# Performance work log

Measured on AMD Instinct MI355X. Metric: run time of the kernel, lower is better.

The kernel has to match this reference:

```python
import jax, jax.numpy as jnp
import numpy as np

HEADS, DIM_HEAD, K_NN, EMB = 4, 64, 16, 256
INNER = HEADS * DIM_HEAD  # 256
POS_HID = 64
ATTN_HID = 4 * DIM_HEAD  # per-head hidden of grouped 1x1 conv MLP


def setup_inputs() -> dict:
    key = jax.random.key(0)
    ks = jax.random.split(key, 16)
    b, n = 2, 4096
    s = 0.05
    inp = {
        "x": jax.random.normal(ks[0], (b, n, EMB), jnp.float32),
        "mask": jnp.ones((b, n), dtype=bool),
        "pos": jax.random.normal(ks[1], (b, n, 3), jnp.float32),
        # to_qkv (no bias)
        "Wqkv": jax.random.normal(ks[2], (EMB, 3 * INNER), jnp.float32) * s,
        # pos_mlp: Linear(3,64) -> ReLU -> Linear(64, inner)
        "Wp1": jax.random.normal(ks[3], (3, POS_HID), jnp.float32) * s,
        "bp1": jax.random.normal(ks[4], (POS_HID,), jnp.float32) * s,
        "Wp2": jax.random.normal(ks[5], (POS_HID, INNER), jnp.float32) * s,
        "bp2": jax.random.normal(ks[6], (INNER,), jnp.float32) * s,
        # attn_mlp: grouped 1x1 convs == per-head linears [h, d_in, d_out]
        "Wa1": jax.random.normal(ks[7], (HEADS, DIM_HEAD, ATTN_HID), jnp.float32) * s,
        "ba1": jax.random.normal(ks[8], (HEADS, ATTN_HID), jnp.float32) * s,
        "Wa2": jax.random.normal(ks[9], (HEADS, ATTN_HID, DIM_HEAD), jnp.float32) * s,
        "ba2": jax.random.normal(ks[10], (HEADS, DIM_HEAD), jnp.float32) * s,
        # to_out
        "Wo": jax.random.normal(ks[11], (INNER, EMB), jnp.float32) * s,
        "bo": jax.random.normal(ks[12], (EMB,), jnp.float32) * s,
    }
    return inp


def reference(x, mask, pos, Wqkv, Wp1, bp1, Wp2, bp2, Wa1, ba1, Wa2, ba2, Wo, bo):
    b, n, _ = x.shape
    h, dh = HEADS, DIM_HEAD

    qkv = x @ Wqkv                              # [b, n, 3*inner]
    q, k, v = jnp.split(qkv, 3, axis=-1)
    to_heads = lambda t: t.reshape(b, n, h, dh).transpose(0, 2, 1, 3)  # [b,h,n,d]
    q, k, v = to_heads(q), to_heads(k), to_heads(v)

    # kNN on pos (per batch, squared euclidean, includes self)
    sq = jnp.sum(pos * pos, axis=-1)
    d2 = sq[:, :, None] + sq[:, None, :] - 2.0 * jnp.einsum('bid,bjd->bij', pos, pos)
    idx = jax.lax.top_k(-d2, K_NN)[1]            # [b, n, K]

    gat_h = jax.vmap(lambda t, i: t[:, i])       # [h,n,d],[n,K] -> [h,n,K,d]
    gat = jax.vmap(lambda t, i: t[i])            # [n,c],[n,K]  -> [n,K,c]

    qg = gat_h(q, idx)                           # [b,h,n,K,d]
    kg = gat_h(k, idx)
    vg = gat_h(v, idx)

    rel = gat(pos, idx) - pos[:, :, None, :]     # [b,n,K,3]
    rpe = jax.nn.relu(rel @ Wp1 + bp1) @ Wp2 + bp2               # [b,n,K,inner]
    rpe = rpe.reshape(b, n, K_NN, h, dh).transpose(0, 3, 1, 2, 4)  # [b,h,n,K,d]

    attn_in = qg - kg + rpe                      # [b,h,n,K,d]
    hid = jax.nn.relu(jnp.einsum('bhnkd,hde->bhnke', attn_in, Wa1)
                      + ba1[None, :, None, None, :])
    sim = (jnp.einsum('bhnke,hed->bhnkd', hid, Wa2)
           + ba2[None, :, None, None, :])        # [b,h,n,K,d]

    mg = jax.vmap(lambda m, i: m[i])(mask, idx)  # [b,n,K]
    pair = (mask[:, :, None] & mg)[:, None, :, :, None]
    sim = jnp.where(pair, sim, -jnp.finfo(sim.dtype).max)

    attn = jax.nn.softmax(sim, axis=3)           # over neighbors j
    # F.normalize over dim=-2 of [b,(h d),i,j] == over the point axis i
    attn = attn / jnp.maximum(jnp.linalg.norm(attn, axis=2, keepdims=True), 1e-12)

    agg = jnp.sum(attn * (vg + rpe), axis=3)     # [b,h,n,d]
    agg = agg.transpose(0, 2, 1, 3).reshape(b, n, h * dh)
    return agg @ Wo + bo
```

## Files before the change

kernel.cpp:

```cpp
#include <hip/hip_runtime.h>
#include <float.h>

typedef unsigned int uint;
typedef unsigned short ushort;

typedef _Float16 f16x8 __attribute__((ext_vector_type(8)));
typedef float f32x4 __attribute__((ext_vector_type(4)));
#define MFMA_F16(A, B, C) __builtin_amdgcn_mfma_f32_16x16x32_f16(A, B, C, 0, 0, 0)

__device__ __forceinline__ ushort f2h(float f) {
    _Float16 h = (_Float16)f;
    return __builtin_bit_cast(ushort, h);
}
__device__ __forceinline__ float h2f(ushort u) {
    _Float16 h = __builtin_bit_cast(_Float16, u);
    return (float)h;
}
__device__ __forceinline__ uint pack2(float a, float b) {
    return (uint)f2h(a) | ((uint)f2h(b) << 16);
}
__device__ __forceinline__ uint pkrtz(float a, float b) {
    return __builtin_bit_cast(uint, __builtin_amdgcn_cvt_pkrtz(a, b));
}
__device__ __forceinline__ f16x8 cast8(uint4 u) {
    return __builtin_bit_cast(f16x8, u);
}

template <int CTRL>
__device__ __forceinline__ void dpp_min(float& v, int& j) {
    int vp = __builtin_amdgcn_update_dpp(__float_as_int(v), __float_as_int(v),
                                         CTRL, 0xF, 0xF, false);
    int jp = __builtin_amdgcn_update_dpp(j, j, CTRL, 0xF, 0xF, false);
    float vf = __int_as_float(vp);
    bool better = (vf < v) || (vf == v && jp < j);
    v = better ? vf : v;
    j = better ? jp : j;
}
__device__ __forceinline__ void wave_min(float& v, int& j) {
    dpp_min<0x121>(v, j);
    dpp_min<0x122>(v, j);
    dpp_min<0x124>(v, j);
    dpp_min<0x128>(v, j);
    float ov = __shfl_xor(v, 16);
    int oj = __shfl_xor(j, 16);
    bool better = (ov < v) || (ov == v && oj < j);
    v = better ? ov : v;
    j = better ? oj : j;
    ov = __shfl_xor(v, 32);
    oj = __shfl_xor(j, 32);
    better = (ov < v) || (ov == v && oj < j);
    v = better ? ov : v;
    j = better ? oj : j;
}

__global__ void prep_kernel(const float* __restrict__ Wqkv, const float* __restrict__ Wa1,
                            const float* __restrict__ Wa2, const float* __restrict__ Wo,
                            const float* __restrict__ Wp2, const float* __restrict__ ba1,
                            ushort* __restrict__ WcatT, ushort* __restrict__ Wa1T,
                            ushort* __restrict__ Wa2T, ushort* __restrict__ WoT,
                            ushort* __restrict__ Wp2T, ushort* __restrict__ ba1p) {
    int t = blockIdx.x * 256 + threadIdx.x;
    {
        int cc2 = t >> 8, kk = t & 255;
        float val;
        if (cc2 < 256) val = Wqkv[kk * 768 + cc2] - Wqkv[kk * 768 + 256 + cc2];
        else           val = Wqkv[kk * 768 + 256 + cc2];
        WcatT[t] = f2h(val);
    }
    if (t < 65536) {
        int hh = t >> 14, r = t & 16383;
        int e = r >> 6, kin = r & 63;
        Wa1T[t] = f2h(Wa1[((size_t)(hh * 64 + kin)) * 256 + e]);
        int d = r >> 8, pos = r & 255;
        int ec = pos >> 5, lg = (pos >> 3) & 3, q = pos & 7;
        int e2 = ec * 32 + ((q >> 2) & 1) * 16 + lg * 4 + (q & 3);
        Wa2T[t] = f2h(Wa2[((size_t)(hh * 256 + e2)) * 64 + d]);
        int c3 = t >> 8, k3 = t & 255;
        WoT[t] = f2h(Wo[k3 * 256 + c3]);
    }
    if (t < 16384) {
        int row = t >> 6, p = t & 63;
        int h = row >> 6, s = row & 63;
        int ct = s >> 4, rr = s & 15;
        int d = (ct >> 1) * 32 + ((rr >> 2) & 3) * 8 + (ct & 1) * 4 + (rr & 3);
        Wp2T[t] = f2h(Wp2[p * 256 + h * 64 + d]);
    }
    if (t < 1024) {
        int h = t >> 8, pos = t & 255;
        int ec = pos >> 5, lg = (pos >> 3) & 3, q = pos & 7;
        int e2 = ec * 32 + ((q >> 2) & 1) * 16 + lg * 4 + (q & 3);
        ba1p[t] = f2h(ba1[h * 256 + e2]);
    }
}

__global__ void pos4_kernel(const float* __restrict__ pos, float4* __restrict__ pos4) {
    int t = blockIdx.x * 256 + threadIdx.x;
    float x = pos[t * 3 + 0], y = pos[t * 3 + 1], z = pos[t * 3 + 2];
    float4 o = {x, y, z, x * x + y * y + z * z};
    pos4[t] = o;
}

template <int MODE>
__global__ __launch_bounds__(256)
void hgemm(const void* __restrict__ Av, const ushort* __restrict__ Bt,
           const float* __restrict__ bias, void* __restrict__ C0v, ushort* __restrict__ C1h) {
    __shared__ ushort Af[64 * 40];
    __shared__ ushort Bf[128 * 40];
    const int tid = threadIdx.x;
    const int l = tid & 63, wv = tid >> 6;
    const int lg = l >> 4, lr = l & 15;
    const int row0 = blockIdx.x * 64, col0 = blockIdx.y * 128;
    const int mrow = (wv >> 1) * 32, ncol = (wv & 1) * 64;
    f32x4 acc[2][4];
#pragma unroll
    for (int mt = 0; mt < 2; ++mt)
#pragma unroll
        for (int nt = 0; nt < 4; ++nt) acc[mt][nt] = (f32x4){0.f, 0.f, 0.f, 0.f};

    for (int kk = 0; kk < 256; kk += 32) {
        if (MODE == 0) {
            const float* A = (const float*)Av;
            int r = tid >> 2, kq = (tid & 3) * 8;
            float4 a0 = *(const float4*)&A[(size_t)(row0 + r) * 256 + kk + kq];
            float4 a1 = *(const float4*)&A[(size_t)(row0 + r) * 256 + kk + kq + 4];
            uint4 u;
            u.x = pack2(a0.x, a0.y); u.y = pack2(a0.z, a0.w);
            u.z = pack2(a1.x, a1.y); u.w = pack2(a1.z, a1.w);
            *(uint4*)&Af[r * 40 + kq] = u;
        } else {
            const ushort* Ah = (const ushort*)Av;
            int r = tid >> 2, kq = (tid & 3) * 8;
            *(uint4*)&Af[r * 40 + kq] = *(const uint4*)&Ah[(size_t)(row0 + r) * 256 + kk + kq];
        }
        {
            int r = tid >> 1, hh = (tid & 1) * 16;
            const uint4* src = (const uint4*)&Bt[(size_t)(col0 + r) * 256 + kk + hh];
            uint4 b0 = src[0], b1 = src[1];
            *(uint4*)&Bf[r * 40 + hh] = b0;
            *(uint4*)&Bf[r * 40 + hh + 8] = b1;
        }
        __syncthreads();
        f16x8 afr[2], bfr[4];
#pragma unroll
        for (int mt = 0; mt < 2; ++mt)
            afr[mt] = *(const f16x8*)&Af[(mrow + mt * 16 + lr) * 40 + lg * 8];
#pragma unroll
        for (int nt = 0; nt < 4; ++nt)
            bfr[nt] = *(const f16x8*)&Bf[(ncol + nt * 16 + lr) * 40 + lg * 8];
#pragma unroll
        for (int mt = 0; mt < 2; ++mt)
#pragma unroll
            for (int nt = 0; nt < 4; ++nt)
                acc[mt][nt] = MFMA_F16(afr[mt], bfr[nt], acc[mt][nt]);
        __syncthreads();
    }
#pragma unroll
    for (int mt = 0; mt < 2; ++mt)
#pragma unroll
        for (int nt = 0; nt < 4; ++nt)
#pragma unroll
            for (int j = 0; j < 4; ++j) {
                int m = row0 + mrow + mt * 16 + lg * 4 + j;
                int n = col0 + ncol + nt * 16 + lr;
                float v = acc[mt][nt][j];
                if (MODE == 1) {
                    ((float*)C0v)[(size_t)m * 256 + n] = v + bias[n];
                } else {
                    int b = m >> 12, i2 = m & 4095;
                    if (n < 256) {
                        int hh = n >> 6, d = n & 63;
                        ((ushort*)C0v)[((size_t)((b * 4 + hh) << 12) + i2) * 64 + d] = f2h(v);
                    } else {
                        int n2 = n - 256;
                        int hh = n2 >> 6, d = n2 & 63;
                        C1h[((size_t)((b * 4 + hh) << 12) + i2) * 64 + d] = f2h(v);
                    }
                }
            }
}

__global__ __launch_bounds__(256, 6)
void knn_kernel(const float4* __restrict__ pos4, int* __restrict__ idx_out) {
    const int tid = threadIdx.x;
    const int lane = tid & 63, wv = tid >> 6;
    const int pblk = blockIdx.x;
    const int b = pblk >> 10;
    const int i = ((pblk & 1023) << 2) + wv;
    const float4* p4 = pos4 + (size_t)b * 4096;
    float4 pi = p4[i];
    float xi = pi.x, yi = pi.y, zi = pi.z, sqi = pi.w;

    float cm4[4];
    int cj4[4];
#pragma unroll
    for (int g = 0; g < 4; ++g) { cm4[g] = FLT_MAX; cj4[g] = 0x7fffffff; }
#pragma unroll 4
    for (int m = 0; m < 64; ++m) {
        int j = m * 64 + lane;
        float4 pj = p4[j];
        float v = sqi + pj.w - 2.f * (xi * pj.x + yi * pj.y + zi * pj.z);
        int g = m & 3;
        bool better = (v < cm4[g]) || (v == cm4[g] && j < cj4[g]);
        cm4[g] = better ? v : cm4[g];
        cj4[g] = better ? j : cj4[g];
    }
    float cm = cm4[0];
    int cj = cj4[0];
#pragma unroll
    for (int g = 1; g < 4; ++g) {
        bool better = (cm4[g] < cm) || (cm4[g] == cm && cj4[g] < cj);
        cm = better ? cm4[g] : cm;
        cj = better ? cj4[g] : cj;
    }

    unsigned long long extr = 0ull;
    int keep = 0;
#pragma unroll 1
    for (int r = 0; r < 16; ++r) {
        float bv = cm;
        int bj = cj;
        wave_min(bv, bj);
        if (lane == r) keep = bj;
        int c = bj & 63;
        int j = lane * 64 + c;
        float4 pj = p4[j];
        float v = sqi + pj.w - 2.f * (xi * pj.x + yi * pj.y + zi * pj.z);
        bool dead = (((extr >> c) & 1ull) != 0ull) | (j == bj);
        if (j == bj) extr |= (1ull << c);
        v = dead ? FLT_MAX : v;
        int nj = j;
        wave_min(v, nj);
        if (lane == c) { cm = v; cj = nj; }
    }
    if (lane < 16)
        idx_out[((size_t)b * 4096 + i) * 16 + lane] = keep;
}

__global__ __launch_bounds__(256)
void attn_mfma(const ushort* __restrict__ qmkh, const ushort* __restrict__ vbufh,
               const float4* __restrict__ pos4, const int* __restrict__ idxb,
               const ushort* __restrict__ Wa1Tg, const ushort* __restrict__ Wa2Tg,
               const ushort* __restrict__ Wp2Tg, const ushort* __restrict__ ba1p,
               const float* __restrict__ ba2,
               const float* __restrict__ Wp1, const float* __restrict__ bp1,
               const float* __restrict__ bp2,
               ushort* __restrict__ prodbuf, float* __restrict__ part) {
    __shared__ ushort scr[4][16 * 88];
    const int tid = threadIdx.x;
    const int l = tid & 63, wv = tid >> 6;
    const int lg = l >> 4, lr = l & 15;
    const int c = blockIdx.x;
    const int h = c >> 8, rc = c & 255, b = rc >> 7, chunk = rc & 127;
    const int bh = b * 4 + h;

    const ushort* w1g = Wa1Tg + (size_t)h * 16384;
    const ushort* w2g = Wa2Tg + (size_t)h * 16384;

    float b2v[4];
#pragma unroll
    for (int dt = 0; dt < 4; ++dt) b2v[dt] = ba2[h * 64 + dt * 16 + lr];

    f16x8 wp2f[4][2];
#pragma unroll
    for (int ct = 0; ct < 4; ++ct)
#pragma unroll
        for (int kt = 0; kt < 2; ++kt)
            wp2f[ct][kt] = *(const f16x8*)&Wp2Tg[(size_t)(h * 64 + ct * 16 + lr) * 64 + kt * 32 + lg * 8];
    f16x8 wp1h[3][2], bp1h[2], bp2h[2];
#pragma unroll
    for (int cc = 0; cc < 3; ++cc)
#pragma unroll
        for (int kt = 0; kt < 2; ++kt) {
            float4 w0 = *(const float4*)&Wp1[cc * 64 + kt * 32 + lg * 8];
            float4 w1 = *(const float4*)&Wp1[cc * 64 + kt * 32 + lg * 8 + 4];
            f16x8 wv8;
            wv8[0] = (_Float16)w0.x; wv8[1] = (_Float16)w0.y;
            wv8[2] = (_Float16)w0.z; wv8[3] = (_Float16)w0.w;
            wv8[4] = (_Float16)w1.x; wv8[5] = (_Float16)w1.y;
            wv8[6] = (_Float16)w1.z; wv8[7] = (_Float16)w1.w;
            wp1h[cc][kt] = wv8;
        }
#pragma unroll
    for (int kt = 0; kt < 2; ++kt) {
        float4 b0 = *(const float4*)&bp1[kt * 32 + lg * 8];
        float4 b1 = *(const float4*)&bp1[kt * 32 + lg * 8 + 4];
        f16x8 bv8;
        bv8[0] = (_Float16)b0.x; bv8[1] = (_Float16)b0.y;
        bv8[2] = (_Float16)b0.z; bv8[3] = (_Float16)b0.w;
        bv8[4] = (_Float16)b1.x; bv8[5] = (_Float16)b1.y;
        bv8[6] = (_Float16)b1.z; bv8[7] = (_Float16)b1.w;
        bp1h[kt] = bv8;
        float4 c0 = *(const float4*)&bp2[h * 64 + kt * 32 + lg * 8];
        float4 c1 = *(const float4*)&bp2[h * 64 + kt * 32 + lg * 8 + 4];
        f16x8 cv8;
        cv8[0] = (_Float16)c0.x; cv8[1] = (_Float16)c0.y;
        cv8[2] = (_Float16)c0.z; cv8[3] = (_Float16)c0.w;
        cv8[4] = (_Float16)c1.x; cv8[5] = (_Float16)c1.y;
        cv8[6] = (_Float16)c1.z; cv8[7] = (_Float16)c1.w;
        bp2h[kt] = cv8;
    }
    const float4* pb4 = pos4 + (size_t)b * 4096;
    const ushort* qbase = qmkh + (size_t)bh * 4096 * 64;
    const ushort* vbase = vbufh + (size_t)bh * 4096 * 64;
    const ushort* b1base = ba1p + h * 256;
    ushort* sw = &scr[wv][0];

    float asq[4][4];
#pragma unroll
    for (int dt = 0; dt < 4; ++dt)
#pragma unroll
        for (int j2 = 0; j2 < 4; ++j2) asq[dt][j2] = 0.f;

    for (int pg = 0; pg < 2; ++pg) {
        const int i0 = chunk * 32 + pg * 16 + wv * 4;
        int jj[4];
        f16x8 ain[4][2], rpef[4][2];
#pragma unroll
        for (int pp = 0; pp < 4; ++pp) {
            int i = i0 + pp;
            int row = ((b << 12) + i) * 16 + lr;
            int j = idxb[row];
            jj[pp] = j;
            float4 pj = pb4[j];
            float4 pi = pb4[i];
            _Float16 rxh = (_Float16)(pj.x - pi.x);
            _Float16 ryh = (_Float16)(pj.y - pi.y);
            _Float16 rzh = (_Float16)(pj.z - pi.z);
            f16x8 hf[2];
#pragma unroll
            for (int kt = 0; kt < 2; ++kt) {
                f16x8 t = bp1h[kt] + rxh * wp1h[0][kt] + ryh * wp1h[1][kt] + rzh * wp1h[2][kt];
#pragma unroll
                for (int q = 0; q < 8; ++q) t[q] = t[q] > (_Float16)0.f ? t[q] : (_Float16)0.f;
                hf[kt] = t;
            }
            f32x4 z4 = {0.f, 0.f, 0.f, 0.f};
            f32x4 racc[4];
#pragma unroll
            for (int ct = 0; ct < 4; ++ct) {
                racc[ct] = MFMA_F16(wp2f[ct][0], hf[0], z4);
                racc[ct] = MFMA_F16(wp2f[ct][1], hf[1], racc[ct]);
            }
            const ushort* qb = qbase + ((size_t)j) * 64 + lg * 8;
#pragma unroll
            for (int kt = 0; kt < 2; ++kt) {
                uint4 rp;
                rp.x = pkrtz(racc[2 * kt][0], racc[2 * kt][1]);
                rp.y = pkrtz(racc[2 * kt][2], racc[2 * kt][3]);
                rp.z = pkrtz(racc[2 * kt + 1][0], racc[2 * kt + 1][1]);
                rp.w = pkrtz(racc[2 * kt + 1][2], racc[2 * kt + 1][3]);
                f16x8 rv = cast8(rp) + bp2h[kt];
                rpef[pp][kt] = rv;
                f16x8 qv = *(const f16x8*)(qb + kt * 32);
                ain[pp][kt] = qv + rv;
            }
        }
        f32x4 acc[4][4];
#pragma unroll
        for (int pp = 0; pp < 4; ++pp)
#pragma unroll
            for (int dt = 0; dt < 4; ++dt) acc[pp][dt] = (f32x4){0.f, 0.f, 0.f, 0.f};

        for (int ec = 0; ec < 8; ++ec) {
            f16x8 A1[2][2], B2f[4];
#pragma unroll
            for (int et = 0; et < 2; ++et)
#pragma unroll
                for (int kt = 0; kt < 2; ++kt)
                    A1[et][kt] = *(const f16x8*)&w1g[(size_t)(ec * 32 + et * 16 + lr) * 64 + kt * 32 + lg * 8];
#pragma unroll
            for (int dt = 0; dt < 4; ++dt)
                B2f[dt] = *(const f16x8*)&w2g[(size_t)(dt * 16 + lr) * 256 + ec * 32 + lg * 8];
            f16x8 b1h = *(const f16x8*)&b1base[ec * 32 + lg * 8];
#pragma unroll
            for (int pp = 0; pp < 4; ++pp) {
                f32x4 z = {0.f, 0.f, 0.f, 0.f};
                f32x4 h0 = MFMA_F16(A1[0][0], ain[pp][0], z);
                h0 = MFMA_F16(A1[0][1], ain[pp][1], h0);
                f32x4 h1 = MFMA_F16(A1[1][0], ain[pp][0], z);
                h1 = MFMA_F16(A1[1][1], ain[pp][1], h1);
                uint4 hp;
                hp.x = pkrtz(h0[0], h0[1]); hp.y = pkrtz(h0[2], h0[3]);
                hp.z = pkrtz(h1[0], h1[1]); hp.w = pkrtz(h1[2], h1[3]);
                f16x8 hv = cast8(hp) + b1h;
#pragma unroll
                for (int q = 0; q < 8; ++q) hv[q] = hv[q] > (_Float16)0.f ? hv[q] : (_Float16)0.f;
#pragma unroll
                for (int dt = 0; dt < 4; ++dt)
                    acc[pp][dt] = MFMA_F16(hv, B2f[dt], acc[pp][dt]);
            }
        }
#pragma unroll
        for (int pp = 0; pp < 4; ++pp) {
            int i = i0 + pp;
            float at[4][4];
#pragma unroll
            for (int dt = 0; dt < 4; ++dt) {
                float v0 = acc[pp][dt][0] + b2v[dt];
                float v1 = acc[pp][dt][1] + b2v[dt];
                float v2 = acc[pp][dt][2] + b2v[dt];
                float v3 = acc[pp][dt][3] + b2v[dt];
                float m = fmaxf(fmaxf(v0, v1), fmaxf(v2, v3));
                m = fmaxf(m, __shfl_xor(m, 16));
                m = fmaxf(m, __shfl_xor(m, 32));
                float e0 = __expf(v0 - m), e1 = __expf(v1 - m);
                float e2 = __expf(v2 - m), e3 = __expf(v3 - m);
                float s = e0 + e1 + e2 + e3;
                s += __shfl_xor(s, 16);
                s += __shfl_xor(s, 32);
                float is = 1.f / s;
                at[dt][0] = e0 * is; at[dt][1] = e1 * is;
                at[dt][2] = e2 * is; at[dt][3] = e3 * is;
                asq[dt][0] += at[dt][0] * at[dt][0];
                asq[dt][1] += at[dt][1] * at[dt][1];
                asq[dt][2] += at[dt][2] * at[dt][2];
                asq[dt][3] += at[dt][3] * at[dt][3];
            }
#pragma unroll
            for (int dt = 0; dt < 4; ++dt) {
                sw[(lg * 4 + 0) * 88 + dt * 16 + lr] = f2h(at[dt][0]);
                sw[(lg * 4 + 1) * 88 + dt * 16 + lr] = f2h(at[dt][1]);
                sw[(lg * 4 + 2) * 88 + dt * 16 + lr] = f2h(at[dt][2]);
                sw[(lg * 4 + 3) * 88 + dt * 16 + lr] = f2h(at[dt][3]);
            }
            const ushort* vb = vbase + (size_t)jj[pp] * 64 + lg * 8;
            ushort* pr = prodbuf + ((size_t)(bh * 4096 + i) * 16 + lr) * 64 + lg * 8;
#pragma unroll
            for (int kt = 0; kt < 2; ++kt) {
                f16x8 atB = *(const f16x8*)&sw[lr * 88 + kt * 32 + lg * 8];
                f16x8 vv = *(const f16x8*)(vb + kt * 32);
                f16x8 p = (vv + rpef[pp][kt]) * atB;
                *(f16x8*)(pr + kt * 32) = p;
            }
        }
    }
    float* scrF = (float*)&scr[0][0];
#pragma unroll
    for (int dt = 0; dt < 4; ++dt) {
        __syncthreads();
#pragma unroll
        for (int j2 = 0; j2 < 4; ++j2)
            scrF[wv * 288 + lr * 18 + lg * 4 + j2] = asq[dt][j2];
        __syncthreads();
        int fr = tid >> 4, fk = tid & 15;
        float s = scrF[fr * 18 + fk] + scrF[288 + fr * 18 + fk] +
                  scrF[576 + fr * 18 + fk] + scrF[864 + fr * 18 + fk];
        part[((size_t)c * 4 + dt) * 256 + tid] = s;
    }
}

__global__ void inv_kernel(const float* __restrict__ part, float* __restrict__ invn) {
    int t = blockIdx.x * 256 + threadIdx.x;
    int bh = t >> 10, f = t & 1023;
    int d = f >> 4, k = f & 15;
    int dt = d >> 4, lr = d & 15;
    int cbase = (bh & 3) * 256 + (bh >> 2) * 128;
    float s = 0.f;
    for (int cc = 0; cc < 128; ++cc)
        s += part[((size_t)(cbase + cc) * 4 + dt) * 256 + lr * 16 + k];
    invn[t] = 1.f / fmaxf(sqrtf(s), 1e-12f);
}

__global__ void finalize_kernel(const ushort* __restrict__ prodbuf, const float* __restrict__ invn,
                                ushort* __restrict__ aggh) {
    int t = blockIdx.x * 256 + threadIdx.x;
    int d = t & 63;
    int i = (t >> 6) & 4095;
    int bh = t >> 18;
    const ushort* pr = prodbuf + ((size_t)(bh * 4096 + i)) * 1024 + d;
    const float* iv = invn + bh * 1024 + d * 16;
    float accv = 0.f;
#pragma unroll
    for (int k = 0; k < 16; ++k)
        accv += h2f(pr[(size_t)k * 64]) * iv[k];
    int hh = bh & 3, bb = bh >> 2;
    aggh[((size_t)(bb * 4096 + i)) * 256 + hh * 64 + d] = f2h(accv);
}

extern "C" void kernel_launch(void* const* d_in, const int* in_sizes, int n_in,
                              void* d_out, int out_size, void* d_ws, size_t ws_size,
                              hipStream_t stream) {
    const float* x    = (const float*)d_in[0];
    const float* pos  = (const float*)d_in[2];
    const float* Wqkv = (const float*)d_in[3];
    const float* Wp1  = (const float*)d_in[4];
    const float* bp1  = (const float*)d_in[5];
    const float* Wp2  = (const float*)d_in[6];
    const float* bp2  = (const float*)d_in[7];
    const float* Wa1  = (const float*)d_in[8];
    const float* ba1  = (const float*)d_in[9];
    const float* Wa2  = (const float*)d_in[10];
    const float* ba2  = (const float*)d_in[11];
    const float* Wo   = (const float*)d_in[12];
    const float* bo   = (const float*)d_in[13];

    char* base = (char*)d_ws;
    size_t off = 0;
    auto carve = [&](size_t bytes) -> char* {
        char* r = base + off;
        off = (off + bytes + 255) & ~(size_t)255;
        return r;
    };
    ushort* qmkh   = (ushort*)carve(4194304);
    ushort* vbufh  = (ushort*)carve(4194304);
    ushort* WcatT  = (ushort*)carve(262144);
    ushort* Wa1Tg  = (ushort*)carve(131072);
    ushort* Wa2Tg  = (ushort*)carve(131072);
    ushort* WoT    = (ushort*)carve(131072);
    ushort* Wp2Tg  = (ushort*)carve(32768);
    ushort* ba1pg  = (ushort*)carve(2048);
    float4* pos4   = (float4*)carve(131072);
    int*    idx    = (int*)carve(524288);
    ushort* prodbuf= (ushort*)carve(67108864);
    float*  part   = (float*)carve(4194304);
    float*  invn   = (float*)carve(32768);
    ushort* aggh   = (ushort*)carve(4194304);

    prep_kernel<<<512, 256, 0, stream>>>(Wqkv, Wa1, Wa2, Wo, Wp2, ba1,
                                         WcatT, Wa1Tg, Wa2Tg, WoT, Wp2Tg, ba1pg);
    pos4_kernel<<<32, 256, 0, stream>>>(pos, pos4);
    hgemm<0><<<dim3(128, 4), 256, 0, stream>>>(x, WcatT, nullptr, qmkh, vbufh);
    knn_kernel<<<2048, 256, 0, stream>>>(pos4, idx);
    attn_mfma<<<1024, 256, 0, stream>>>(qmkh, vbufh, pos4, idx, Wa1Tg, Wa2Tg, Wp2Tg, ba1pg,
                                        ba2, Wp1, bp1, bp2, prodbuf, part);
    inv_kernel<<<32, 256, 0, stream>>>(part, invn);
    finalize_kernel<<<8192, 256, 0, stream>>>(prodbuf, invn, aggh);
    hgemm<1><<<dim3(128, 2), 256, 0, stream>>>(aggh, WoT, bo, d_out, nullptr);
}
```

Baseline: 213.5 us.

## Keep top-2 per kNN column and stage attention MLP weights in LDS

The kNN kernel now tracks the two best candidates per column group instead of one. Most of the 16 extraction rounds can then promote the runner-up without rescanning the column, and a rescan happens only when both candidates are used up. The attention kernel copies the per-head Wa1/Wa2 fp16 weights into padded shared memory once per block, so the inner loop reads them from LDS instead of global/L2. The cost is more registers and compare logic in kNN, about 71KB more LDS per block (which may lower occupancy), and a startup sync.

```diff
diff --git a/kernel.cpp b/kernel.cpp
--- a/kernel.cpp
+++ b/kernel.cpp
@@ -189,48 +189,75 @@
     const float4* p4 = pos4 + (size_t)b * 4096;
     float4 pi = p4[i];
     float xi = pi.x, yi = pi.y, zi = pi.z, sqi = pi.w;
-
-    float cm4[4];
-    int cj4[4];
-#pragma unroll
-    for (int g = 0; g < 4; ++g) { cm4[g] = FLT_MAX; cj4[g] = 0x7fffffff; }
+    const int SENT = 0x7fffffff;
+
+    float v1[4], v2[4];
+    int j1[4], j2[4];
+#pragma unroll
+    for (int g = 0; g < 4; ++g) { v1[g] = FLT_MAX; v2[g] = FLT_MAX; j1[g] = SENT; j2[g] = SENT; }
 #pragma unroll 4
     for (int m = 0; m < 64; ++m) {
         int j = m * 64 + lane;
         float4 pj = p4[j];
         float v = sqi + pj.w - 2.f * (xi * pj.x + yi * pj.y + zi * pj.z);
         int g = m & 3;
-        bool better = (v < cm4[g]) || (v == cm4[g] && j < cj4[g]);
-        cm4[g] = better ? v : cm4[g];
-        cj4[g] = better ? j : cj4[g];
-    }
-    float cm = cm4[0];
-    int cj = cj4[0];
-#pragma unroll
-    for (int g = 1; g < 4; ++g) {
-        bool better = (cm4[g] < cm) || (cm4[g] == cm && cj4[g] < cj);
-        cm = better ? cm4[g] : cm;
-        cj = better ? cj4[g] : cj;
-    }
+        bool bb1 = (v < v1[g]) || (v == v1[g] && j < j1[g]);
+        bool bb2 = (v < v2[g]) || (v == v2[g] && j < j2[g]);
+        float nv2 = bb1 ? v1[g] : (bb2 ? v : v2[g]);
+        int   nj2 = bb1 ? j1[g] : (bb2 ? j : j2[g]);
+        v1[g] = bb1 ? v : v1[g];
+        j1[g] = bb1 ? j : j1[g];
+        v2[g] = nv2;
+        j2[g] = nj2;
+    }
+    auto mergef = [](float& a1, int& aj1, float& a2, int& aj2,
+                     float b1v, int bj1, float b2v, int bj2) {
+        bool aFirst = (a1 < b1v) || (a1 == b1v && aj1 < bj1);
+        float r1 = aFirst ? a1 : b1v;
+        int rj1 = aFirst ? aj1 : bj1;
+        float cand = aFirst ? a2 : b2v;
+        int candj = aFirst ? aj2 : bj2;
+        float oth = aFirst ? b1v : a1;
+        int othj = aFirst ? bj1 : aj1;
+        bool second = (cand < oth) || (cand == oth && candj < othj);
+        a1 = r1; aj1 = rj1;
+        a2 = second ? cand : oth;
+        aj2 = second ? candj : othj;
+    };
+    mergef(v1[0], j1[0], v2[0], j2[0], v1[1], j1[1], v2[1], j2[1]);
+    mergef(v1[2], j1[2], v2[2], j2[2], v1[3], j1[3], v2[3], j2[3]);
+    mergef(v1[0], j1[0], v2[0], j2[0], v1[2], j1[2], v2[2], j2[2]);
+    float c1v = v1[0], c2v = v2[0];
+    int c1j = j1[0], c2j = j2[0];
 
     unsigned long long extr = 0ull;
     int keep = 0;
 #pragma unroll 1
     for (int r = 0; r < 16; ++r) {
-        float bv = cm;
-        int bj = cj;
+        float bv = c1v;
+        int bj = c1j;
         wave_min(bv, bj);
         if (lane == r) keep = bj;
         int c = bj & 63;
-        int j = lane * 64 + c;
-        float4 pj = p4[j];
-        float v = sqi + pj.w - 2.f * (xi * pj.x + yi * pj.y + zi * pj.z);
-        bool dead = (((extr >> c) & 1ull) != 0ull) | (j == bj);
-        if (j == bj) extr |= (1ull << c);
-        v = dead ? FLT_MAX : v;
-        int nj = j;
-        wave_min(v, nj);
-        if (lane == c) { cm = v; cj = nj; }
+        if (lane == (bj >> 6)) extr |= (1ull << c);
+        if (lane == c) {
+            c1v = c2v; c1j = c2j;
+            c2v = FLT_MAX; c2j = SENT;
+        }
+        unsigned long long need = __ballot(lane == c && c1j == SENT);
+        if (need) {
+            int j = lane * 64 + c;
+            float4 pj = p4[j];
+            float v = sqi + pj.w - 2.f * (xi * pj.x + yi * pj.y + zi * pj.z);
+            bool dead = (((extr >> c) & 1ull) != 0ull);
+            v = dead ? FLT_MAX : v;
+            float w1 = v; int wj1 = j;
+            wave_min(w1, wj1);
+            float w2 = (j == wj1) ? FLT_MAX : v;
+            int wj2 = (j == wj1) ? SENT : j;
+            wave_min(w2, wj2);
+            if (lane == c) { c1v = w1; c1j = wj1; c2v = w2; c2j = wj2; }
+        }
     }
     if (lane < 16)
         idx_out[((size_t)b * 4096 + i) * 16 + lane] = keep;
@@ -245,6 +272,8 @@
                const float* __restrict__ Wp1, const float* __restrict__ bp1,
                const float* __restrict__ bp2,
                ushort* __restrict__ prodbuf, float* __restrict__ part) {
+    __shared__ ushort W1[256 * 72];
+    __shared__ ushort W2[64 * 264];
     __shared__ ushort scr[4][16 * 88];
     const int tid = threadIdx.x;
     const int l = tid & 63, wv = tid >> 6;
@@ -253,8 +282,21 @@
     const int h = c >> 8, rc = c & 255, b = rc >> 7, chunk = rc & 127;
     const int bh = b * 4 + h;
 
-    const ushort* w1g = Wa1Tg + (size_t)h * 16384;
-    const ushort* w2g = Wa2Tg + (size_t)h * 16384;
+    {
+        const uint4* g1 = (const uint4*)(Wa1Tg + (size_t)h * 16384);
+        const uint4* g2 = (const uint4*)(Wa2Tg + (size_t)h * 16384);
+#pragma unroll
+        for (int it = 0; it < 8; ++it) {
+            int ci = it * 256 + tid;
+            *(uint4*)&W1[(ci >> 3) * 72 + (ci & 7) * 8] = g1[ci];
+        }
+#pragma unroll
+        for (int it = 0; it < 8; ++it) {
+            int ci = it * 256 + tid;
+            *(uint4*)&W2[(ci >> 5) * 264 + (ci & 31) * 8] = g2[ci];
+        }
+    }
+    __syncthreads();
 
     float b2v[4];
 #pragma unroll
@@ -367,10 +409,10 @@
             for (int et = 0; et < 2; ++et)
 #pragma unroll
                 for (int kt = 0; kt < 2; ++kt)
-                    A1[et][kt] = *(const f16x8*)&w1g[(size_t)(ec * 32 + et * 16 + lr) * 64 + kt * 32 + lg * 8];
+                    A1[et][kt] = *(const f16x8*)&W1[(ec * 32 + et * 16 + lr) * 72 + kt * 32 + lg * 8];
 #pragma unroll
             for (int dt = 0; dt < 4; ++dt)
-                B2f[dt] = *(const f16x8*)&w2g[(size_t)(dt * 16 + lr) * 256 + ec * 32 + lg * 8];
+                B2f[dt] = *(const f16x8*)&W2[(dt * 16 + lr) * 264 + ec * 32 + lg * 8];
             f16x8 b1h = *(const f16x8*)&b1base[ec * 32 + lg * 8];
 #pragma unroll
             for (int pp = 0; pp < 4; ++pp) {
```

Result: faster. 190.8 us (-10.6%).
